# Optimization experiments

Hardware: AMD Instinct MI355X
Metric: run time of the kernel (lower is better)

## Reference

```python
import jax, jax.numpy as jnp
import numpy as np

D_MODEL, D_INNER, D_STATE, D_CONV, DT_RANK = 512, 1024, 64, 4, 32
B, L = 2, 1000
EPS = 1e-5


def _rmsnorm(x, w):
    return x * jax.lax.rsqrt(jnp.mean(x * x, axis=-1, keepdims=True) + EPS) * w


def _causal_dwconv(x, w, b):
    # x: (B, L, Di); w: (Di, K) depthwise causal conv, output length L
    xT = jnp.transpose(x, (0, 2, 1))  # (B, Di, L)
    y = jax.lax.conv_general_dilated(
        xT, w[:, None, :], window_strides=(1,), padding=[(D_CONV - 1, 0)],
        dimension_numbers=('NCH', 'OIH', 'NCH'), feature_group_count=D_INNER)
    return jnp.transpose(y + b[None, :, None], (0, 2, 1))


def _selective_scan(u, dt, A, Bm, Cm):
    # u, dt: (B, L, Di); A: (Di, N); Bm, Cm: (B, L, N)
    def step(h, inp):
        dt_t, B_t, C_t, u_t = inp
        dA = jnp.exp(dt_t[..., None] * A)                       # (B, Di, N)
        h = dA * h + (dt_t * u_t)[..., None] * B_t[:, None, :]  # state update
        y = jnp.einsum('bdn,bn->bd', h, C_t)
        return h, y
    xs = (jnp.swapaxes(dt, 0, 1), jnp.swapaxes(Bm, 0, 1),
          jnp.swapaxes(Cm, 0, 1), jnp.swapaxes(u, 0, 1))
    h0 = jnp.zeros((u.shape[0], D_INNER, D_STATE), u.dtype)
    _, ys = jax.lax.scan(step, h0, xs)
    return jnp.swapaxes(ys, 0, 1)  # (B, L, Di)


def _mamba_layer(x, norm_w, in_proj, conv_w, conv_b, x_proj, dt_w, dt_b, A_log, Dp, out_proj):
    # mamba-ssm Block with fused_add_norm=False, n_layer=1:
    # residual = x; h = mixer(rmsnorm(x)); block output pair merges to h + x
    h = _rmsnorm(x, norm_w)
    xz = jnp.einsum('bld,ed->ble', h, in_proj)        # (B, L, 2*Di)
    xc, z = jnp.split(xz, 2, axis=-1)
    xc = jax.nn.silu(_causal_dwconv(xc, conv_w, conv_b))
    x_dbl = jnp.einsum('bld,ed->ble', xc, x_proj)     # (B, L, dt_rank + 2N)
    dt, Bm, Cm = jnp.split(x_dbl, [DT_RANK, DT_RANK + D_STATE], axis=-1)
    dt = jax.nn.softplus(jnp.einsum('blr,dr->bld', dt, dt_w) + dt_b)
    A = -jnp.exp(A_log)
    y = _selective_scan(xc, dt, A, Bm, Cm)
    y = (y + xc * Dp) * jax.nn.silu(z)
    return jnp.einsum('bld,ed->ble', y, out_proj) + x


def _forward(x,
             f_norm_w, f_in_proj, f_conv_w, f_conv_b, f_x_proj, f_dt_w, f_dt_b, f_A_log, f_D, f_out_proj,
             b_norm_w, b_in_proj, b_conv_w, b_conv_b, b_x_proj, b_dt_w, b_dt_b, b_A_log, b_D, b_out_proj):
    res_f = _mamba_layer(x, f_norm_w, f_in_proj, f_conv_w, f_conv_b, f_x_proj,
                         f_dt_w, f_dt_b, f_A_log, f_D, f_out_proj)
    res_b = _mamba_layer(jnp.flip(x, 1), b_norm_w, b_in_proj, b_conv_w, b_conv_b,
                         b_x_proj, b_dt_w, b_dt_b, b_A_log, b_D, b_out_proj)
    return res_f + jnp.flip(res_b, 1)  # bidirectional_merging='add'


def setup_inputs() -> dict:
    key = jax.random.key(0)
    ks = iter(jax.random.split(key, 32))
    def nrm(shape, s=0.02):
        return jax.random.normal(next(ks), shape, jnp.float32) * s
    inp = {'x': jax.random.normal(next(ks), (B, L, D_MODEL), jnp.float32)}
    for p in ('f', 'b'):
        inp[p + '_norm_w'] = jnp.ones((D_MODEL,), jnp.float32)
        inp[p + '_in_proj'] = nrm((2 * D_INNER, D_MODEL))
        inp[p + '_conv_w'] = nrm((D_INNER, D_CONV), 0.1)
        inp[p + '_conv_b'] = nrm((D_INNER,), 0.1)
        inp[p + '_x_proj'] = nrm((DT_RANK + 2 * D_STATE, D_INNER))
        inp[p + '_dt_w'] = nrm((D_INNER, DT_RANK), 0.1)
        inp[p + '_dt_b'] = jnp.full((D_INNER,), float(np.log(np.expm1(0.01))), jnp.float32)
        inp[p + '_A_log'] = jnp.log(jnp.tile(jnp.arange(1, D_STATE + 1, dtype=jnp.float32), (D_INNER, 1)))
        inp[p + '_D'] = jnp.ones((D_INNER,), jnp.float32)
        inp[p + '_out_proj'] = nrm((D_MODEL, D_INNER))
    return inp


def reference(x,
              f_norm_w, f_in_proj, f_conv_w, f_conv_b, f_x_proj, f_dt_w, f_dt_b, f_A_log, f_D, f_out_proj,
              b_norm_w, b_in_proj, b_conv_w, b_conv_b, b_x_proj, b_dt_w, b_dt_b, b_A_log, b_D, b_out_proj):
    return _forward(x,
                    f_norm_w, f_in_proj, f_conv_w, f_conv_b, f_x_proj, f_dt_w, f_dt_b, f_A_log, f_D, f_out_proj,
                    b_norm_w, b_in_proj, b_conv_w, b_conv_b, b_x_proj, b_dt_w, b_dt_b, b_A_log, b_D, b_out_proj)
```

## Files before the change

### kernel.cpp

```cpp
#include <hip/hip_runtime.h>
#include <hip/hip_bf16.h>
#include <math.h>

#define DM   512
#define DI   1024
#define NS   64
#define RDT  32
#define BB   2
#define LL   1000
#define MROWS (BB*LL)

typedef __attribute__((ext_vector_type(8))) short bf16x8;
typedef __attribute__((ext_vector_type(4))) float f32x4;

__device__ __forceinline__ unsigned short f2bf(float f) {
    unsigned u = __builtin_bit_cast(unsigned, f);
    u = (u + 0x7FFF + ((u >> 16) & 1)) >> 16;
    return (unsigned short)u;
}

__device__ __forceinline__ float bcast_lane(float v, int lane) {
    return __builtin_bit_cast(float,
        __builtin_amdgcn_readlane(__builtin_bit_cast(int, v), lane));
}

__global__ __launch_bounds__(256)
void rmsnorm_k(const float* __restrict__ x,
               const float* __restrict__ nw0, const float* __restrict__ nw1,
               unsigned short* __restrict__ xnb0, unsigned short* __restrict__ xnb1) {
    int row = blockIdx.x;
    int tid = threadIdx.x;
    const float* xr = x + (size_t)row * DM;
    float2 v = *(const float2*)(xr + tid * 2);
    float ss = v.x * v.x + v.y * v.y;
    #pragma unroll
    for (int off = 32; off; off >>= 1) ss += __shfl_xor(ss, off, 64);
    __shared__ float red[4];
    if ((tid & 63) == 0) red[tid >> 6] = ss;
    __syncthreads();
    float tot = red[0] + red[1] + red[2] + red[3];
    float scale = rsqrtf(tot / (float)DM + 1e-5f);
    float2 w0 = *(const float2*)(nw0 + tid * 2);
    float2 w1 = *(const float2*)(nw1 + tid * 2);
    short2 o0, o1;
    o0.x = (short)f2bf(v.x * scale * w0.x);
    o0.y = (short)f2bf(v.y * scale * w0.y);
    o1.x = (short)f2bf(v.x * scale * w1.x);
    o1.y = (short)f2bf(v.y * scale * w1.y);
    *(short2*)(xnb0 + (size_t)row * DM + tid * 2) = o0;
    *(short2*)(xnb1 + (size_t)row * DM + tid * 2) = o1;
}

__global__ __launch_bounds__(256)
void cvt2_k(const float* __restrict__ in0, const float* __restrict__ in1,
            unsigned short* __restrict__ out0, unsigned short* __restrict__ out1,
            int n4) {
    int idx = blockIdx.x * 256 + threadIdx.x;
    if (idx >= n4) return;
    const float* in = blockIdx.y ? in1 : in0;
    unsigned short* out = blockIdx.y ? out1 : out0;
    float4 v = *(const float4*)(in + (size_t)idx * 4);
    short4 o;
    o.x = (short)f2bf(v.x); o.y = (short)f2bf(v.y);
    o.z = (short)f2bf(v.z); o.w = (short)f2bf(v.w);
    *(short4*)(out + (size_t)idx * 4) = o;
}

__global__ __launch_bounds__(256, 2)
void gemm1_mfma(const unsigned short* __restrict__ xnb0,
                const unsigned short* __restrict__ xnb1,
                const unsigned short* __restrict__ wib0,
                const unsigned short* __restrict__ wib1,
                float* __restrict__ xz0, float* __restrict__ xz1)
{
    __shared__ __align__(16) unsigned short As[128 * 40];
    __shared__ __align__(16) unsigned short Bs[128 * 40];
    int dir = blockIdx.z;
    const unsigned short* A = dir ? xnb1 : xnb0;
    const unsigned short* W = dir ? wib1 : wib0;
    float* C = dir ? xz1 : xz0;
    int n0 = blockIdx.x * 128, m0 = blockIdx.y * 128;
    int tid = threadIdx.x;
    int wv = tid >> 6, lane = tid & 63;
    int wr = wv >> 1, wc = wv & 1;
    int fl = lane & 15, kg = lane >> 4;

    f32x4 acc[4][4];
    #pragma unroll
    for (int i = 0; i < 4; i++)
        #pragma unroll
        for (int j = 0; j < 4; j++) acc[i][j] = (f32x4){0.f, 0.f, 0.f, 0.f};

    int sr = tid >> 2, cg = tid & 3;
    for (int k0 = 0; k0 < 512; k0 += 32) {
        #pragma unroll
        for (int i = 0; i < 2; i++) {
            int row = sr + i * 64;
            int m = m0 + row;
            float4 av = make_float4(0.f, 0.f, 0.f, 0.f);
            if (m < MROWS) {
                int rs = m;
                if (dir) { int b = m / LL, t = m % LL; rs = b * LL + (LL - 1 - t); }
                av = *(const float4*)(A + (size_t)rs * 512 + k0 + cg * 8);
            }
            *(float4*)(&As[row * 40 + cg * 8]) = av;
            float4 wv4 = *(const float4*)(W + (size_t)(n0 + row) * 512 + k0 + cg * 8);
            *(float4*)(&Bs[row * 40 + cg * 8]) = wv4;
        }
        __syncthreads();
        bf16x8 af[4], bf[4];
        #pragma unroll
        for (int fr = 0; fr < 4; fr++)
            af[fr] = *(const bf16x8*)(&As[(wr * 64 + fr * 16 + fl) * 40 + kg * 8]);
        #pragma unroll
        for (int fc = 0; fc < 4; fc++)
            bf[fc] = *(const bf16x8*)(&Bs[(wc * 64 + fc * 16 + fl) * 40 + kg * 8]);
        #pragma unroll
        for (int fr = 0; fr < 4; fr++)
            #pragma unroll
            for (int fc = 0; fc < 4; fc++)
                acc[fr][fc] = __builtin_amdgcn_mfma_f32_16x16x32_bf16(
                    af[fr], bf[fc], acc[fr][fc], 0, 0, 0);
        __syncthreads();
    }
    #pragma unroll
    for (int fr = 0; fr < 4; fr++)
        #pragma unroll
        for (int fc = 0; fc < 4; fc++)
            #pragma unroll
            for (int j = 0; j < 4; j++) {
                int m = m0 + wr * 64 + fr * 16 + kg * 4 + j;
                if (m < MROWS) {
                    int n = n0 + wc * 64 + fc * 16 + fl;
                    C[(size_t)m * 2048 + n] = acc[fr][fc][j];
                }
            }
}

__global__ __launch_bounds__(256, 2)
void gemm_out_mfma(const unsigned short* __restrict__ ygb0,
                   const unsigned short* __restrict__ ygb1,
                   const unsigned short* __restrict__ wob0,
                   const unsigned short* __restrict__ wob1,
                   float* __restrict__ partial)
{
    __shared__ __align__(16) unsigned short As[64 * 40];
    __shared__ __align__(16) unsigned short Bs[64 * 40];
    int dir = blockIdx.z;
    const unsigned short* A = dir ? ygb1 : ygb0;
    const unsigned short* W = dir ? wob1 : wob0;
    float* P = partial + (size_t)dir * MROWS * 512;
    int n0 = blockIdx.x * 64, m0 = blockIdx.y * 64;
    int tid = threadIdx.x;
    int wv = tid >> 6, lane = tid & 63;
    int wr = wv >> 1, wc = wv & 1;
    int fl = lane & 15, kg = lane >> 4;

    f32x4 acc[2][2];
    #pragma unroll
    for (int i = 0; i < 2; i++)
        #pragma unroll
        for (int j = 0; j < 2; j++) acc[i][j] = (f32x4){0.f, 0.f, 0.f, 0.f};

    int sr = tid >> 2, cg = tid & 3;
    for (int k0 = 0; k0 < 1024; k0 += 32) {
        int m = m0 + sr;
        float4 av = make_float4(0.f, 0.f, 0.f, 0.f);
        if (m < MROWS)
            av = *(const float4*)(A + (size_t)m * 1024 + k0 + cg * 8);
        *(float4*)(&As[sr * 40 + cg * 8]) = av;
        float4 wv4 = *(const float4*)(W + (size_t)(n0 + sr) * 1024 + k0 + cg * 8);
        *(float4*)(&Bs[sr * 40 + cg * 8]) = wv4;
        __syncthreads();
        bf16x8 af[2], bf[2];
        #pragma unroll
        for (int fr = 0; fr < 2; fr++)
            af[fr] = *(const bf16x8*)(&As[(wr * 32 + fr * 16 + fl) * 40 + kg * 8]);
        #pragma unroll
        for (int fc = 0; fc < 2; fc++)
            bf[fc] = *(const bf16x8*)(&Bs[(wc * 32 + fc * 16 + fl) * 40 + kg * 8]);
        #pragma unroll
        for (int fr = 0; fr < 2; fr++)
            #pragma unroll
            for (int fc = 0; fc < 2; fc++)
                acc[fr][fc] = __builtin_amdgcn_mfma_f32_16x16x32_bf16(
                    af[fr], bf[fc], acc[fr][fc], 0, 0, 0);
        __syncthreads();
    }
    #pragma unroll
    for (int fr = 0; fr < 2; fr++)
        #pragma unroll
        for (int fc = 0; fc < 2; fc++)
            #pragma unroll
            for (int j = 0; j < 4; j++) {
                int m = m0 + wr * 32 + fr * 16 + kg * 4 + j;
                if (m < MROWS) {
                    int n = n0 + wc * 32 + fc * 16 + fl;
                    P[(size_t)m * 512 + n] = acc[fr][fc][j];
                }
            }
}

__global__ __launch_bounds__(256)
void reduce_out_k(const float* __restrict__ x, const float* __restrict__ partial,
                  float* __restrict__ out)
{
    int idx = blockIdx.x * 256 + threadIdx.x;
    if (idx >= MROWS * 128) return;
    int m = idx >> 7, q = idx & 127;
    int b = m / LL, t = m % LL;
    int fm = b * LL + (LL - 1 - t);
    const float* p0 = partial;
    const float* p1 = partial + (size_t)MROWS * 512;
    float4 xv = *(const float4*)(x  + (size_t)m  * 512 + q * 4);
    float4 a  = *(const float4*)(p0 + (size_t)m  * 512 + q * 4);
    float4 c  = *(const float4*)(p1 + (size_t)fm * 512 + q * 4);
    float4 o;
    o.x = 2.f * xv.x + a.x + c.x;
    o.y = 2.f * xv.y + a.y + c.y;
    o.z = 2.f * xv.z + a.z + c.z;
    o.w = 2.f * xv.w + a.w + c.w;
    *(float4*)(out + (size_t)m * 512 + q * 4) = o;
}

__global__ __launch_bounds__(256)
void conv_silu_k(const float* __restrict__ xz0, const float* __restrict__ xz1,
                 const float* __restrict__ cw0, const float* __restrict__ cw1,
                 const float* __restrict__ cb0, const float* __restrict__ cb1,
                 float* __restrict__ xcT0, float* __restrict__ xcT1)
{
    __shared__ float Ls[64 * 65];
    int dirb = blockIdx.z;
    int dir = dirb >> 1, b = dirb & 1;
    int d0 = blockIdx.x * 64, t0 = blockIdx.y * 64;
    int tid = threadIdx.x;
    int dl = tid & 63, tg = tid >> 6;

    const float* in = (dir ? xz1 : xz0) + (size_t)b * LL * 2048;
    const float* cw = dir ? cw1 : cw0;
    const float* cb = dir ? cb1 : cb0;
    float*      xcT = dir ? xcT1 : xcT0;

    float4 w4 = ((const float4*)cw)[d0 + dl];
    float bias = cb[d0 + dl];

    int ts = t0 + tg * 16;
    float x3 = 0.f, x2 = 0.f, x1 = 0.f;
    if (ts - 3 >= 0 && ts - 3 < LL) x3 = in[(size_t)(ts - 3) * 2048 + d0 + dl];
    if (ts - 2 >= 0 && ts - 2 < LL) x2 = in[(size_t)(ts - 2) * 2048 + d0 + dl];
    if (ts - 1 >= 0 && ts - 1 < LL) x1 = in[(size_t)(ts - 1) * 2048 + d0 + dl];

    #pragma unroll
    for (int i = 0; i < 16; i++) {
        int t = ts + i;
        float x0v = (t < LL) ? in[(size_t)t * 2048 + d0 + dl] : 0.f;
        float a = bias + x3 * w4.x + x2 * w4.y + x1 * w4.z + x0v * w4.w;
        float s = a / (1.f + __expf(-a));
        Ls[dl * 65 + tg * 16 + i] = s;
        x3 = x2; x2 = x1; x1 = x0v;
    }
    __syncthreads();
    int tl = tid & 63, dg = tid >> 6;
    #pragma unroll
    for (int i = 0; i < 16; i++) {
        int dd = dg * 16 + i;
        int t = t0 + tl;
        if (t < LL)
            xcT[((size_t)(b * 1024) + d0 + dd) * LL + t] = Ls[dd * 65 + tl];
    }
}

__global__ __launch_bounds__(256)
void gemm_xp_k(const float* __restrict__ xcT0, const float* __restrict__ xcT1,
               const float* __restrict__ xp0, const float* __restrict__ xp1,
               float* __restrict__ xd0, float* __restrict__ xd1,
               float* __restrict__ bct)
{
    __shared__ float As[16 * 68];
    __shared__ float Ws[16 * 68];
    __shared__ float T[64 * 67];
    int dirb = blockIdx.z;
    int dir = dirb >> 1, b = dirb & 1;
    const float* xcT = (dir ? xcT1 : xcT0) + (size_t)b * 1024 * LL;
    const float* W   = dir ? xp1 : xp0;
    float*       C   = (dir ? xd1 : xd0) + (size_t)b * LL * 160;
    int n0 = blockIdx.x * 64, t0 = blockIdx.y * 64;
    int tid = threadIdx.x;
    int tx = tid & 15, ty = tid >> 4;

    float acc[4][4] = {};

    for (int k0 = 0; k0 < 1024; k0 += 16) {
        {
            int kk = tid & 15, mq = tid >> 4;
            float4 v = make_float4(0.f, 0.f, 0.f, 0.f);
            if (t0 + mq * 4 + 3 < LL)
                v = *(const float4*)(xcT + (size_t)(k0 + kk) * LL + t0 + mq * 4);
            *(float4*)(As + kk * 68 + mq * 4) = v;
        }
        {
            int row = tid >> 2, q = tid & 3;
            float4 v = make_float4(0.f, 0.f, 0.f, 0.f);
            if (n0 + row < 160)
                v = *(const float4*)(W + (size_t)(n0 + row) * 1024 + k0 + q * 4);
            Ws[(q * 4 + 0) * 68 + row] = v.x;
            Ws[(q * 4 + 1) * 68 + row] = v.y;
            Ws[(q * 4 + 2) * 68 + row] = v.z;
            Ws[(q * 4 + 3) * 68 + row] = v.w;
        }
        __syncthreads();
        #pragma unroll
        for (int k = 0; k < 16; k++) {
            float4 a = *(const float4*)(As + k * 68 + ty * 4);
            float4 w = *(const float4*)(Ws + k * 68 + tx * 4);
            float av[4] = {a.x, a.y, a.z, a.w};
            float wvv[4] = {w.x, w.y, w.z, w.w};
            #pragma unroll
            for (int i = 0; i < 4; i++)
                #pragma unroll
                for (int j = 0; j < 4; j++)
                    acc[i][j] = fmaf(av[i], wvv[j], acc[i][j]);
        }
        __syncthreads();
    }

    if (n0 == 0) {
        #pragma unroll
        for (int i = 0; i < 4; i++) {
            int t = t0 + ty * 4 + i;
            if (t >= LL) continue;
            #pragma unroll
            for (int j = 0; j < 4; j++) {
                int n = tx * 4 + j;
                C[(size_t)t * 160 + n] = acc[i][j];
            }
        }
    }

    #pragma unroll
    for (int i = 0; i < 4; i++)
        #pragma unroll
        for (int j = 0; j < 4; j++)
            T[(tx * 4 + j) * 67 + ty * 4 + i] = acc[i][j];
    __syncthreads();
    int tl = tid & 63, ng = tid >> 6;
    #pragma unroll
    for (int i = 0; i < 16; i++) {
        int nl = ng * 16 + i;
        int n = n0 + nl;
        int t = t0 + tl;
        if (n >= 32 && n < 160 && t < LL)
            bct[((size_t)dirb * 128 + (n - 32)) * LL + t] = T[nl * 67 + tl];
    }
}

__global__ __launch_bounds__(256)
void gemm_dt_k(const float* __restrict__ xd0, const float* __restrict__ xd1,
               const float* __restrict__ w0, const float* __restrict__ w1,
               const float* __restrict__ bb0, const float* __restrict__ bb1,
               float* __restrict__ dtT0, float* __restrict__ dtT1)
{
    __shared__ float As[64 * 33];
    __shared__ float Ws[32 * 68];
    __shared__ float T[64 * 67];
    int dirb = blockIdx.z;
    int dir = dirb >> 1, b = dirb & 1;
    const float* xd = (dir ? xd1 : xd0) + (size_t)b * LL * 160;
    const float* W  = dir ? w1 : w0;
    const float* bi = dir ? bb1 : bb0;
    float*      dtT = (dir ? dtT1 : dtT0) + (size_t)b * 1024 * LL;
    int n0 = blockIdx.x * 64, t0 = blockIdx.y * 64;
    int tid = threadIdx.x;
    int tx = tid & 15, ty = tid >> 4;

    #pragma unroll
    for (int i = 0; i < 2; i++) {
        int j = tid + 256 * i;
        int row = j >> 3, q = j & 7;
        float4 v = make_float4(0.f, 0.f, 0.f, 0.f);
        if (t0 + row < LL)
            v = *(const float4*)(xd + (size_t)(t0 + row) * 160 + q * 4);
        As[row * 33 + q * 4 + 0] = v.x;
        As[row * 33 + q * 4 + 1] = v.y;
        As[row * 33 + q * 4 + 2] = v.z;
        As[row * 33 + q * 4 + 3] = v.w;
        float4 wv = *(const float4*)(W + (size_t)(n0 + row) * 32 + q * 4);
        Ws[(q * 4 + 0) * 68 + row] = wv.x;
        Ws[(q * 4 + 1) * 68 + row] = wv.y;
        Ws[(q * 4 + 2) * 68 + row] = wv.z;
        Ws[(q * 4 + 3) * 68 + row] = wv.w;
    }
    __syncthreads();

    float acc[4][4] = {};
    #pragma unroll 8
    for (int k = 0; k < 32; k++) {
        float4 w = *(const float4*)(Ws + k * 68 + tx * 4);
        float wvv[4] = {w.x, w.y, w.z, w.w};
        float av[4];
        #pragma unroll
        for (int i = 0; i < 4; i++) av[i] = As[(ty * 4 + i) * 33 + k];
        #pragma unroll
        for (int i = 0; i < 4; i++)
            #pragma unroll
            for (int j = 0; j < 4; j++)
                acc[i][j] = fmaf(av[i], wvv[j], acc[i][j]);
    }
    __syncthreads();

    #pragma unroll
    for (int i = 0; i < 4; i++) {
        #pragma unroll
        for (int j = 0; j < 4; j++) {
            int n = tx * 4 + j;
            float v = acc[i][j] + bi[n0 + n];
            v = (v > 20.f) ? v : log1pf(__expf(v));
            T[n * 67 + ty * 4 + i] = v;
        }
    }
    __syncthreads();

    int tl = tid & 63, ng = tid >> 6;
    #pragma unroll
    for (int i = 0; i < 16; i++) {
        int nl = ng * 16 + i;
        int t = t0 + tl;
        if (t < LL)
            dtT[(size_t)(n0 + nl) * LL + t] = T[nl * 67 + tl];
    }
}

__global__ __launch_bounds__(256)
void scan_k(float* __restrict__ dtT0, float* __restrict__ dtT1,
            const float* __restrict__ ucT0, const float* __restrict__ ucT1,
            const float* __restrict__ bct,
            const float* __restrict__ Al0, const float* __restrict__ Al1,
            const float* __restrict__ Dc0, const float* __restrict__ Dc1)
{
    __shared__ float Bs[64 * 34];
    __shared__ float Cs[64 * 34];
    __shared__ float Pt[4][16 * 66];
    int dirb = blockIdx.y;
    int dir = dirb >> 1, b = dirb & 1;
    int wid = threadIdx.x >> 6, lane = threadIdx.x & 63;
    int d = blockIdx.x * 4 + wid;
    float* Pw = Pt[wid];

    float*       dtT = (dir ? dtT1 : dtT0);
    const float* ucT = (dir ? ucT1 : ucT0);
    const float* Al  = dir ? Al1 : Al0;
    const float* Dc  = dir ? Dc1 : Dc0;

    float a  = -__expf(Al[d * 64 + lane]) * 1.44269504f;
    float Dp = Dc[d];
    float h  = 0.f;
    size_t chan = ((size_t)(b * 1024 + d)) * LL;
    const float* Bg = bct + (size_t)dirb * 128 * LL;

    int srow = threadIdx.x >> 2;
    int scol = (threadIdx.x & 3) * 8;
    int tl16 = lane & 15, qq = lane >> 4;
    const float* Prow = Pw + tl16 * 66 + qq * 16;

    float4 rb0, rb1, rc0, rc1;
    float dta = 0.f, ua = 0.f;
    {
        const float* Bp = Bg + (size_t)srow * LL + scol;
        const float* Cp = Bg + (size_t)(srow + 64) * LL + scol;
        rb0 = *(const float4*)(Bp);     rb1 = *(const float4*)(Bp + 4);
        rc0 = *(const float4*)(Cp);     rc1 = *(const float4*)(Cp + 4);
        if (lane < 32) {
            dta = dtT[chan + lane];
            ua  = ucT[chan + lane];
        }
    }

    for (int t0 = 0; t0 < LL; t0 += 32) {
        int rem = min(32, LL - t0);
        __syncthreads();
        *(float4*)(&Bs[srow * 34 + scol])     = rb0;
        *(float4*)(&Bs[srow * 34 + scol + 4]) = rb1;
        *(float4*)(&Cs[srow * 34 + scol])     = rc0;
        *(float4*)(&Cs[srow * 34 + scol + 4]) = rc1;
        float dcur = dta, ucur = ua;
        float wsc  = dcur * ucur;
        __syncthreads();

        if (t0 + 32 < LL) {
            const float* Bp = Bg + (size_t)srow * LL + (t0 + 32) + scol;
            const float* Cp = Bg + (size_t)(srow + 64) * LL + (t0 + 32) + scol;
            rb0 = *(const float4*)(Bp);     rb1 = *(const float4*)(Bp + 4);
            rc0 = *(const float4*)(Cp);     rc1 = *(const float4*)(Cp + 4);
            if (lane < min(32, LL - t0 - 32)) {
                dta = dtT[chan + t0 + 32 + lane];
                ua  = ucT[chan + t0 + 32 + lane];
            }
        }

        for (int sec = 0; sec < 2; sec++) {
            int sbase = sec * 16;
            int steps = rem - sbase;
            if (steps <= 0) break;
            if (steps > 16) steps = 16;
            if (steps < 16) {
                for (int i = steps; i < 16; i++) Pw[i * 66 + lane] = 0.f;
            }
            int ngr = (steps + 7) >> 3;
            for (int g = 0; g < ngr; g++) {
                int tb = sbase + g * 8;
                float4 B0 = *(const float4*)(&Bs[lane * 34 + tb]);
                float4 B1 = *(const float4*)(&Bs[lane * 34 + tb + 4]);
                float4 C0 = *(const float4*)(&Cs[lane * 34 + tb]);
                float4 C1 = *(const float4*)(&Cs[lane * 34 + tb + 4]);
                #pragma unroll
                for (int i = 0; i < 8; i++) {
                    float dtv = bcast_lane(dcur, tb + i);
                    float w   = bcast_lane(wsc,  tb + i);
                    float dA  = exp2f(dtv * a);
                    float Bn  = (i < 4) ? B0[i] : B1[i - 4];
                    float Cn  = (i < 4) ? C0[i] : C1[i - 4];
                    h = fmaf(dA, h, w * Bn);
                    Pw[(g * 8 + i) * 66 + lane] = h * Cn;
                }
            }
            float s = 0.f;
            #pragma unroll
            for (int j = 0; j < 8; j++) {
                float2 v = *(const float2*)(Prow + j * 2);
                s += v.x + v.y;
            }
#if __has_builtin(__builtin_amdgcn_permlane32_swap)
            {
                unsigned aa = __builtin_bit_cast(unsigned, s);
                auto r = __builtin_amdgcn_permlane32_swap(aa, aa, false, false);
                s = __builtin_bit_cast(float, (unsigned)r[0]) +
                    __builtin_bit_cast(float, (unsigned)r[1]);
            }
#else
            s += __shfl_xor(s, 32, 64);
#endif
#if __has_builtin(__builtin_amdgcn_permlane16_swap)
            {
                unsigned aa = __builtin_bit_cast(unsigned, s);
                auto r = __builtin_amdgcn_permlane16_swap(aa, aa, false, false);
                s = __builtin_bit_cast(float, (unsigned)r[0]) +
                    __builtin_bit_cast(float, (unsigned)r[1]);
            }
#else
            s += __shfl_xor(s, 16, 64);
#endif
            float uf = __shfl(ucur, sbase + tl16, 64);
            s = fmaf(uf, Dp, s);
            if (lane < steps)
                dtT[chan + t0 + sbase + lane] = s;
        }
    }
}

__global__ __launch_bounds__(256)
void gate_k(const float* __restrict__ yT0, const float* __restrict__ yT1,
            const float* __restrict__ xz0, const float* __restrict__ xz1,
            unsigned short* __restrict__ yg0, unsigned short* __restrict__ yg1)
{
    __shared__ float Ls[64 * 65];
    int dirb = blockIdx.z;
    int dir = dirb >> 1, b = dirb & 1;
    int d0 = blockIdx.x * 64, t0 = blockIdx.y * 64;
    int tid = threadIdx.x;
    const float* yT = (dir ? yT1 : yT0) + (size_t)b * 1024 * LL;
    const float* xz = (dir ? xz1 : xz0) + (size_t)b * LL * 2048;
    unsigned short* yg = dir ? yg1 : yg0;

    int tl = tid & 63, dg = tid >> 6;
    #pragma unroll
    for (int i = 0; i < 16; i++) {
        int dd = dg * 16 + i;
        int t = t0 + tl;
        float v = (t < LL) ? yT[(size_t)(d0 + dd) * LL + t] : 0.f;
        Ls[dd * 65 + tl] = v;
    }
    __syncthreads();
    int dcol = tid & 63, tg = tid >> 6;
    #pragma unroll
    for (int i = 0; i < 16; i++) {
        int t = t0 + tg * 16 + i;
        if (t >= LL) continue;
        float z = xz[(size_t)t * 2048 + 1024 + d0 + dcol];
        float y = Ls[dcol * 65 + tg * 16 + i];
        float s = z / (1.f + __expf(-z));
        yg[((size_t)(b * LL + t)) * 1024 + d0 + dcol] = f2bf(y * s);
    }
}

extern "C" void kernel_launch(void* const* d_in, const int* in_sizes, int n_in,
                              void* d_out, int out_size, void* d_ws, size_t ws_size,
                              hipStream_t stream) {
    const float* x = (const float*)d_in[0];
    const float* P[2][10];
    for (int dir = 0; dir < 2; dir++)
        for (int i = 0; i < 10; i++)
            P[dir][i] = (const float*)d_in[1 + dir * 10 + i];

    float* ws = (float*)d_ws;
    float* xz0   = ws;
    float* xz1   = ws + 4096000;
    float* xcT0  = ws + 8192000;
    float* xcT1  = ws + 10240000;
    float* dtT0  = ws + 12288000;
    float* dtT1  = ws + 14336000;
    float* xdbl0 = ws + 16384000;
    float* xdbl1 = ws + 16704000;
    unsigned short* xnb0 = (unsigned short*)(ws + 17024000);
    unsigned short* xnb1 = (unsigned short*)(ws + 17280000);
    unsigned short* wib0 = (unsigned short*)dtT0;
    unsigned short* wib1 = (unsigned short*)dtT1;
    unsigned short* ygb0 = (unsigned short*)xcT0;
    unsigned short* ygb1 = (unsigned short*)xcT1;
    unsigned short* wob0 = (unsigned short*)dtT0;
    unsigned short* wob1 = (unsigned short*)dtT1;
    float* partial = xz0;
    float* bct = (float*)d_out;
    float* out = (float*)d_out;

    rmsnorm_k<<<MROWS, 256, 0, stream>>>(x, P[0][0], P[1][0], xnb0, xnb1);

    cvt2_k<<<dim3(1024, 2), 256, 0, stream>>>(P[0][1], P[1][1], wib0, wib1, 262144);

    gemm1_mfma<<<dim3(16, 16, 2), 256, 0, stream>>>(
        xnb0, xnb1, wib0, wib1, xz0, xz1);

    conv_silu_k<<<dim3(16, 16, 4), 256, 0, stream>>>(
        xz0, xz1, P[0][2], P[1][2], P[0][3], P[1][3], xcT0, xcT1);

    gemm_xp_k<<<dim3(3, 16, 4), 256, 0, stream>>>(
        xcT0, xcT1, P[0][4], P[1][4], xdbl0, xdbl1, bct);

    gemm_dt_k<<<dim3(16, 16, 4), 256, 0, stream>>>(
        xdbl0, xdbl1, P[0][5], P[1][5], P[0][6], P[1][6], dtT0, dtT1);

    scan_k<<<dim3(256, 4), 256, 0, stream>>>(
        dtT0, dtT1, xcT0, xcT1, bct,
        P[0][7], P[1][7], P[0][8], P[1][8]);

    gate_k<<<dim3(16, 16, 4), 256, 0, stream>>>(
        dtT0, dtT1, xz0, xz1, ygb0, ygb1);

    cvt2_k<<<dim3(512, 2), 256, 0, stream>>>(P[0][9], P[1][9], wob0, wob1, 131072);

    gemm_out_mfma<<<dim3(8, 32, 2), 256, 0, stream>>>(
        ygb0, ygb1, wob0, wob1, partial);

    reduce_out_k<<<1000, 256, 0, stream>>>(x, partial, out);
}
```

Baseline: 316.0 us.

## Move x_proj GEMM to bf16 MFMA and enlarge out-proj GEMM tiles

Replaces the fp32 FMA x_proj GEMM with a bf16 MFMA kernel. The conv kernel now also writes a row-major bf16 copy of the conv output, and the x_proj weights are converted to bf16 in a new step. The xdbl buffer shrinks to hold only the dt part, and the workspace is reshuffled so the new bf16 buffers fit. The out-projection MFMA GEMM moves from 64x64 to 128x128 tiles for more data reuse per block, which also means far fewer blocks. The x_proj grid is small (64 blocks), and its bf16 inputs lower precision for the dt, B and C terms.

```diff
diff --git a/kernel.cpp b/kernel.cpp
--- a/kernel.cpp
+++ b/kernel.cpp
@@ -144,58 +144,62 @@
                    const unsigned short* __restrict__ wob1,
                    float* __restrict__ partial)
 {
-    __shared__ __align__(16) unsigned short As[64 * 40];
-    __shared__ __align__(16) unsigned short Bs[64 * 40];
+    __shared__ __align__(16) unsigned short As[128 * 40];
+    __shared__ __align__(16) unsigned short Bs[128 * 40];
     int dir = blockIdx.z;
     const unsigned short* A = dir ? ygb1 : ygb0;
     const unsigned short* W = dir ? wob1 : wob0;
     float* P = partial + (size_t)dir * MROWS * 512;
-    int n0 = blockIdx.x * 64, m0 = blockIdx.y * 64;
+    int n0 = blockIdx.x * 128, m0 = blockIdx.y * 128;
     int tid = threadIdx.x;
     int wv = tid >> 6, lane = tid & 63;
     int wr = wv >> 1, wc = wv & 1;
     int fl = lane & 15, kg = lane >> 4;
 
-    f32x4 acc[2][2];
-    #pragma unroll
-    for (int i = 0; i < 2; i++)
-        #pragma unroll
-        for (int j = 0; j < 2; j++) acc[i][j] = (f32x4){0.f, 0.f, 0.f, 0.f};
+    f32x4 acc[4][4];
+    #pragma unroll
+    for (int i = 0; i < 4; i++)
+        #pragma unroll
+        for (int j = 0; j < 4; j++) acc[i][j] = (f32x4){0.f, 0.f, 0.f, 0.f};
 
     int sr = tid >> 2, cg = tid & 3;
     for (int k0 = 0; k0 < 1024; k0 += 32) {
-        int m = m0 + sr;
-        float4 av = make_float4(0.f, 0.f, 0.f, 0.f);
-        if (m < MROWS)
-            av = *(const float4*)(A + (size_t)m * 1024 + k0 + cg * 8);
-        *(float4*)(&As[sr * 40 + cg * 8]) = av;
-        float4 wv4 = *(const float4*)(W + (size_t)(n0 + sr) * 1024 + k0 + cg * 8);
-        *(float4*)(&Bs[sr * 40 + cg * 8]) = wv4;
-        __syncthreads();
-        bf16x8 af[2], bf[2];
-        #pragma unroll
-        for (int fr = 0; fr < 2; fr++)
-            af[fr] = *(const bf16x8*)(&As[(wr * 32 + fr * 16 + fl) * 40 + kg * 8]);
-        #pragma unroll
-        for (int fc = 0; fc < 2; fc++)
-            bf[fc] = *(const bf16x8*)(&Bs[(wc * 32 + fc * 16 + fl) * 40 + kg * 8]);
-        #pragma unroll
-        for (int fr = 0; fr < 2; fr++)
+        #pragma unroll
+        for (int i = 0; i < 2; i++) {
+            int row = sr + i * 64;
+            int m = m0 + row;
+            float4 av = make_float4(0.f, 0.f, 0.f, 0.f);
+            if (m < MROWS)
+                av = *(const float4*)(A + (size_t)m * 1024 + k0 + cg * 8);
+            *(float4*)(&As[row * 40 + cg * 8]) = av;
+            float4 wv4 = *(const float4*)(W + (size_t)(n0 + row) * 1024 + k0 + cg * 8);
+            *(float4*)(&Bs[row * 40 + cg * 8]) = wv4;
+        }
+        __syncthreads();
+        bf16x8 af[4], bf[4];
+        #pragma unroll
+        for (int fr = 0; fr < 4; fr++)
+            af[fr] = *(const bf16x8*)(&As[(wr * 64 + fr * 16 + fl) * 40 + kg * 8]);
+        #pragma unroll
+        for (int fc = 0; fc < 4; fc++)
+            bf[fc] = *(const bf16x8*)(&Bs[(wc * 64 + fc * 16 + fl) * 40 + kg * 8]);
+        #pragma unroll
+        for (int fr = 0; fr < 4; fr++)
             #pragma unroll
-            for (int fc = 0; fc < 2; fc++)
+            for (int fc = 0; fc < 4; fc++)
                 acc[fr][fc] = __builtin_amdgcn_mfma_f32_16x16x32_bf16(
                     af[fr], bf[fc], acc[fr][fc], 0, 0, 0);
         __syncthreads();
     }
     #pragma unroll
-    for (int fr = 0; fr < 2; fr++)
-        #pragma unroll
-        for (int fc = 0; fc < 2; fc++)
+    for (int fr = 0; fr < 4; fr++)
+        #pragma unroll
+        for (int fc = 0; fc < 4; fc++)
             #pragma unroll
             for (int j = 0; j < 4; j++) {
-                int m = m0 + wr * 32 + fr * 16 + kg * 4 + j;
+                int m = m0 + wr * 64 + fr * 16 + kg * 4 + j;
                 if (m < MROWS) {
-                    int n = n0 + wc * 32 + fc * 16 + fl;
+                    int n = n0 + wc * 64 + fc * 16 + fl;
                     P[(size_t)m * 512 + n] = acc[fr][fc][j];
                 }
             }
@@ -227,7 +231,8 @@
 void conv_silu_k(const float* __restrict__ xz0, const float* __restrict__ xz1,
                  const float* __restrict__ cw0, const float* __restrict__ cw1,
                  const float* __restrict__ cb0, const float* __restrict__ cb1,
-                 float* __restrict__ xcT0, float* __restrict__ xcT1)
+                 float* __restrict__ xcT0, float* __restrict__ xcT1,
+                 unsigned short* __restrict__ xcb0, unsigned short* __restrict__ xcb1)
 {
     __shared__ float Ls[64 * 65];
     int dirb = blockIdx.z;
@@ -240,6 +245,7 @@
     const float* cw = dir ? cw1 : cw0;
     const float* cb = dir ? cb1 : cb0;
     float*      xcT = dir ? xcT1 : xcT0;
+    unsigned short* xcb = dir ? xcb1 : xcb0;
 
     float4 w4 = ((const float4*)cw)[d0 + dl];
     float bias = cb[d0 + dl];
@@ -257,6 +263,8 @@
         float a = bias + x3 * w4.x + x2 * w4.y + x1 * w4.z + x0v * w4.w;
         float s = a / (1.f + __expf(-a));
         Ls[dl * 65 + tg * 16 + i] = s;
+        if (t < LL)
+            xcb[((size_t)(b * LL + t)) * 1024 + d0 + dl] = f2bf(s);
         x3 = x2; x2 = x1; x1 = x0v;
     }
     __syncthreads();
@@ -270,87 +278,68 @@
     }
 }
 
-__global__ __launch_bounds__(256)
-void gemm_xp_k(const float* __restrict__ xcT0, const float* __restrict__ xcT1,
-               const float* __restrict__ xp0, const float* __restrict__ xp1,
-               float* __restrict__ xd0, float* __restrict__ xd1,
-               float* __restrict__ bct)
-{
-    __shared__ float As[16 * 68];
-    __shared__ float Ws[16 * 68];
-    __shared__ float T[64 * 67];
-    int dirb = blockIdx.z;
+__global__ __launch_bounds__(256, 2)
+void gemm_xp_mfma(const unsigned short* __restrict__ xcb0,
+                  const unsigned short* __restrict__ xcb1,
+                  const unsigned short* __restrict__ xpb0,
+                  const unsigned short* __restrict__ xpb1,
+                  float* __restrict__ xd0, float* __restrict__ xd1,
+                  float* __restrict__ bct)
+{
+    __shared__ __align__(16) unsigned short As[64 * 40];
+    __shared__ __align__(16) unsigned short Ws[160 * 40];
+    int dirb = blockIdx.y;
     int dir = dirb >> 1, b = dirb & 1;
-    const float* xcT = (dir ? xcT1 : xcT0) + (size_t)b * 1024 * LL;
-    const float* W   = dir ? xp1 : xp0;
-    float*       C   = (dir ? xd1 : xd0) + (size_t)b * LL * 160;
-    int n0 = blockIdx.x * 64, t0 = blockIdx.y * 64;
+    const unsigned short* A = (dir ? xcb1 : xcb0) + (size_t)b * LL * 1024;
+    const unsigned short* W = dir ? xpb1 : xpb0;
+    float* xd = (dir ? xd1 : xd0) + (size_t)b * LL * 32;
+    float* bc = bct + (size_t)dirb * 128 * LL;
+    int m0 = blockIdx.x * 64;
     int tid = threadIdx.x;
-    int tx = tid & 15, ty = tid >> 4;
-
-    float acc[4][4] = {};
-
-    for (int k0 = 0; k0 < 1024; k0 += 16) {
+    int wv = tid >> 6, lane = tid & 63;
+    int fl = lane & 15, kg = lane >> 4;
+
+    f32x4 acc[10];
+    #pragma unroll
+    for (int f = 0; f < 10; f++) acc[f] = (f32x4){0.f, 0.f, 0.f, 0.f};
+
+    int sr = tid >> 2, cg = tid & 3;
+    for (int k0 = 0; k0 < 1024; k0 += 32) {
         {
-            int kk = tid & 15, mq = tid >> 4;
-            float4 v = make_float4(0.f, 0.f, 0.f, 0.f);
-            if (t0 + mq * 4 + 3 < LL)
-                v = *(const float4*)(xcT + (size_t)(k0 + kk) * LL + t0 + mq * 4);
-            *(float4*)(As + kk * 68 + mq * 4) = v;
-        }
-        {
-            int row = tid >> 2, q = tid & 3;
-            float4 v = make_float4(0.f, 0.f, 0.f, 0.f);
-            if (n0 + row < 160)
-                v = *(const float4*)(W + (size_t)(n0 + row) * 1024 + k0 + q * 4);
-            Ws[(q * 4 + 0) * 68 + row] = v.x;
-            Ws[(q * 4 + 1) * 68 + row] = v.y;
-            Ws[(q * 4 + 2) * 68 + row] = v.z;
-            Ws[(q * 4 + 3) * 68 + row] = v.w;
-        }
-        __syncthreads();
-        #pragma unroll
-        for (int k = 0; k < 16; k++) {
-            float4 a = *(const float4*)(As + k * 68 + ty * 4);
-            float4 w = *(const float4*)(Ws + k * 68 + tx * 4);
-            float av[4] = {a.x, a.y, a.z, a.w};
-            float wvv[4] = {w.x, w.y, w.z, w.w};
-            #pragma unroll
-            for (int i = 0; i < 4; i++)
-                #pragma unroll
-                for (int j = 0; j < 4; j++)
-                    acc[i][j] = fmaf(av[i], wvv[j], acc[i][j]);
-        }
-        __syncthreads();
-    }
-
-    if (n0 == 0) {
-        #pragma unroll
-        for (int i = 0; i < 4; i++) {
-            int t = t0 + ty * 4 + i;
+            int t = m0 + sr;
+            float4 av = make_float4(0.f, 0.f, 0.f, 0.f);
+            if (t < LL)
+                av = *(const float4*)(A + (size_t)t * 1024 + k0 + cg * 8);
+            *(float4*)(&As[sr * 40 + cg * 8]) = av;
+        }
+        #pragma unroll
+        for (int it = 0; it < 3; it++) {
+            int row = sr + it * 64;
+            if (row < 160) {
+                float4 wv4 = *(const float4*)(W + (size_t)row * 1024 + k0 + cg * 8);
+                *(float4*)(&Ws[row * 40 + cg * 8]) = wv4;
+            }
+        }
+        __syncthreads();
+        bf16x8 af = *(const bf16x8*)(&As[(wv * 16 + fl) * 40 + kg * 8]);
+        #pragma unroll
+        for (int f = 0; f < 10; f++) {
+            bf16x8 bf = *(const bf16x8*)(&Ws[(f * 16 + fl) * 40 + kg * 8]);
+            acc[f] = __builtin_amdgcn_mfma_f32_16x16x32_bf16(af, bf, acc[f], 0, 0, 0);
+        }
+        __syncthreads();
+    }
+
+    #pragma unroll
+    for (int f = 0; f < 10; f++) {
+        int n = f * 16 + fl;
+        #pragma unroll
+        for (int j = 0; j < 4; j++) {
+            int t = m0 + wv * 16 + kg * 4 + j;
             if (t >= LL) continue;
-            #pragma unroll
-            for (int j = 0; j < 4; j++) {
-                int n = tx * 4 + j;
-                C[(size_t)t * 160 + n] = acc[i][j];
-            }
-        }
-    }
-
-    #pragma unroll
-    for (int i = 0; i < 4; i++)
-        #pragma unroll
-        for (int j = 0; j < 4; j++)
-            T[(tx * 4 + j) * 67 + ty * 4 + i] = acc[i][j];
-    __syncthreads();
-    int tl = tid & 63, ng = tid >> 6;
-    #pragma unroll
-    for (int i = 0; i < 16; i++) {
-        int nl = ng * 16 + i;
-        int n = n0 + nl;
-        int t = t0 + tl;
-        if (n >= 32 && n < 160 && t < LL)
-            bct[((size_t)dirb * 128 + (n - 32)) * LL + t] = T[nl * 67 + tl];
+            if (f < 2) xd[(size_t)t * 32 + n] = acc[f][j];
+            else       bc[(size_t)(n - 32) * LL + t] = acc[f][j];
+        }
     }
 }
 
@@ -365,7 +354,7 @@
     __shared__ float T[64 * 67];
     int dirb = blockIdx.z;
     int dir = dirb >> 1, b = dirb & 1;
-    const float* xd = (dir ? xd1 : xd0) + (size_t)b * LL * 160;
+    const float* xd = (dir ? xd1 : xd0) + (size_t)b * LL * 32;
     const float* W  = dir ? w1 : w0;
     const float* bi = dir ? bb1 : bb0;
     float*      dtT = (dir ? dtT1 : dtT0) + (size_t)b * 1024 * LL;
@@ -379,7 +368,7 @@
         int row = j >> 3, q = j & 7;
         float4 v = make_float4(0.f, 0.f, 0.f, 0.f);
         if (t0 + row < LL)
-            v = *(const float4*)(xd + (size_t)(t0 + row) * 160 + q * 4);
+            v = *(const float4*)(xd + (size_t)(t0 + row) * 32 + q * 4);
         As[row * 33 + q * 4 + 0] = v.x;
         As[row * 33 + q * 4 + 1] = v.y;
         As[row * 33 + q * 4 + 2] = v.z;
@@ -609,15 +598,19 @@
     float* dtT0  = ws + 12288000;
     float* dtT1  = ws + 14336000;
     float* xdbl0 = ws + 16384000;
-    float* xdbl1 = ws + 16704000;
+    float* xdbl1 = ws + 16448000;
     unsigned short* xnb0 = (unsigned short*)(ws + 17024000);
     unsigned short* xnb1 = (unsigned short*)(ws + 17280000);
-    unsigned short* wib0 = (unsigned short*)dtT0;
-    unsigned short* wib1 = (unsigned short*)dtT1;
+    unsigned short* wib0 = (unsigned short*)(ws + 14336000);
+    unsigned short* wib1 = (unsigned short*)(ws + 14860288);
+    unsigned short* xcb0 = (unsigned short*)(ws + 12288000);
+    unsigned short* xcb1 = (unsigned short*)(ws + 13312000);
+    unsigned short* xpb0 = (unsigned short*)(ws + 17024000);
+    unsigned short* xpb1 = (unsigned short*)(ws + 17280000);
     unsigned short* ygb0 = (unsigned short*)xcT0;
     unsigned short* ygb1 = (unsigned short*)xcT1;
     unsigned short* wob0 = (unsigned short*)dtT0;
-    unsigned short* wob1 = (unsigned short*)dtT1;
+    unsigned short* wob1 = (unsigned short*)(dtT0 + 262144);
     float* partial = xz0;
     float* bct = (float*)d_out;
     float* out = (float*)d_out;
@@ -629,11 +622,13 @@
     gemm1_mfma<<<dim3(16, 16, 2), 256, 0, stream>>>(
         xnb0, xnb1, wib0, wib1, xz0, xz1);
 
+    cvt2_k<<<dim3(160, 2), 256, 0, stream>>>(P[0][4], P[1][4], xpb0, xpb1, 40960);
+
     conv_silu_k<<<dim3(16, 16, 4), 256, 0, stream>>>(
-        xz0, xz1, P[0][2], P[1][2], P[0][3], P[1][3], xcT0, xcT1);
-
-    gemm_xp_k<<<dim3(3, 16, 4), 256, 0, stream>>>(
-        xcT0, xcT1, P[0][4], P[1][4], xdbl0, xdbl1, bct);
+        xz0, xz1, P[0][2], P[1][2], P[0][3], P[1][3], xcT0, xcT1, xcb0, xcb1);
+
+    gemm_xp_mfma<<<dim3(16, 4), 256, 0, stream>>>(
+        xcb0, xcb1, xpb0, xpb1, xdbl0, xdbl1, bct);
 
     gemm_dt_k<<<dim3(16, 16, 4), 256, 0, stream>>>(
         xdbl0, xdbl1, P[0][5], P[1][5], P[0][6], P[1][6], dtT0, dtT1);
@@ -647,7 +642,7 @@
 
     cvt2_k<<<dim3(512, 2), 256, 0, stream>>>(P[0][9], P[1][9], wob0, wob1, 131072);
 
-    gemm_out_mfma<<<dim3(8, 32, 2), 256, 0, stream>>>(
+    gemm_out_mfma<<<dim3(4, 16, 2), 256, 0, stream>>>(
         ygb0, ygb1, wob0, wob1, partial);
 
     reduce_out_k<<<1000, 256, 0, stream>>>(x, partial, out);
```

Measured after the change: 296.7 us. -6.1%, faster.
